# Optimization experiments

Hardware: AMD Instinct MI355X
Metric: run time of the kernel (lower is better)

## Reference

```python
import jax, jax.numpy as jnp
import numpy as np

N_NODES = 100000
N_EDGES = 1600000
IN_DIM = 128
HID = 128
HEADS = 8
NEG_SLOPE = 0.2  # PyG GATConv default


def _gat_layer(x, src, dst, W, a_src, a_dst, bias, heads, n_nodes):
    """One PyG-style GATConv (concat=True). src/dst already include self-loops."""
    out_ch = W.shape[1] // heads
    h = (x @ W).reshape(n_nodes, heads, out_ch)          # [N, H, C]
    alpha_s = jnp.sum(h * a_src, axis=-1)                # [N, H]
    alpha_d = jnp.sum(h * a_dst, axis=-1)                # [N, H]
    e = jax.nn.leaky_relu(alpha_s[src] + alpha_d[dst], negative_slope=NEG_SLOPE)  # [E, H]
    # segment softmax over destination nodes (stable; self-loops guarantee nonempty segments)
    m = jax.lax.stop_gradient(jax.ops.segment_max(e, dst, num_segments=n_nodes))
    ex = jnp.exp(e - m[dst])
    s = jax.ops.segment_sum(ex, dst, num_segments=n_nodes)
    alpha = ex / s[dst]                                  # [E, H]
    msg = h[src] * alpha[:, :, None]                     # [E, H, C]
    out = jax.ops.segment_sum(msg, dst, num_segments=n_nodes)  # [N, H, C]
    return out.reshape(n_nodes, heads * out_ch) + bias


def setup_inputs() -> dict:
    key = jax.random.key(0)
    ks = jax.random.split(key, 12)
    c1 = HID // HEADS  # per-head channels of layer 1
    g = lambda k, shape, fan_in: jax.random.normal(k, shape, dtype=jnp.float32) * (1.0 / np.sqrt(fan_in))
    return {
        "x": jax.random.normal(ks[0], (N_NODES, IN_DIM), dtype=jnp.float32),
        "edge_index": jax.random.randint(ks[1], (2, N_EDGES), 0, N_NODES, dtype=jnp.int32),
        "W1": g(ks[2], (IN_DIM, HEADS * c1), IN_DIM),
        "a_src1": g(ks[3], (HEADS, c1), c1),
        "a_dst1": g(ks[4], (HEADS, c1), c1),
        "b1": jnp.zeros((HEADS * c1,), dtype=jnp.float32),
        "W2": g(ks[5], (HID, HID), HID),
        "a_src2": g(ks[6], (1, HID), HID),
        "a_dst2": g(ks[7], (1, HID), HID),
        "b2": jnp.zeros((HID,), dtype=jnp.float32),
    }


def reference(x, edge_index, W1, a_src1, a_dst1, b1, W2, a_src2, a_dst2, b2):
    n = x.shape[0]
    loops = jnp.arange(n, dtype=edge_index.dtype)  # add_self_loops=True (PyG default)
    src = jnp.concatenate([edge_index[0], loops])
    dst = jnp.concatenate([edge_index[1], loops])
    h = _gat_layer(x, src, dst, W1, a_src1, a_dst1, b1, HEADS, n)
    h = jax.nn.elu(h)  # inter-layer ELU; dropout p=0.0 is a no-op
    out = _gat_layer(h, src, dst, W2, a_src2, a_dst2, b2, 1, n)
    return out
```

## Files before the change

kernel.cpp:

```cpp
#include <hip/hip_runtime.h>
#include <hip/hip_bf16.h>
#include <math.h>

#define NEG_SLOPE 0.2f

typedef _Float16 half8 __attribute__((ext_vector_type(8)));
typedef _Float16 half4 __attribute__((ext_vector_type(4)));
typedef _Float16 half2v __attribute__((ext_vector_type(2)));
typedef float f32x4 __attribute__((ext_vector_type(4)));

__device__ __forceinline__ float lrelu(float x){ return fmaxf(x, NEG_SLOPE * x); }

__global__ void hist_kernel(const int* __restrict__ dst, int E,
                            int* __restrict__ deg, int rangeSize){
  const int x   = blockIdx.x & 7;
  const int gb  = blockIdx.x >> 3;
  const int nGB = gridDim.x >> 3;
  const int lo = x * rangeSize, hi = lo + rangeSize;
  const int stride = nGB * blockDim.x;
  for (int i = gb * blockDim.x + threadIdx.x; i < E; i += stride){
    int d = dst[i];
    if (d >= lo && d < hi) atomicAdd(&deg[d], 1);
  }
}

__global__ void scan1_kernel(const int* __restrict__ deg, int N,
                             int* __restrict__ rowptr, int* __restrict__ bsum){
  __shared__ int sdata[256];
  int t = threadIdx.x;
  int base = blockIdx.x * 1024;
  int v[4];
  int run = 0;
#pragma unroll
  for (int j = 0; j < 4; ++j){
    int idx = base + t*4 + j;
    int d = (idx < N) ? deg[idx] : 0;
    run += d;
    v[j] = run;
  }
  sdata[t] = run;
  __syncthreads();
  for (int off = 1; off < 256; off <<= 1){
    int x = (t >= off) ? sdata[t - off] : 0;
    __syncthreads();
    sdata[t] += x;
    __syncthreads();
  }
  int prev = (t > 0) ? sdata[t-1] : 0;
#pragma unroll
  for (int j = 0; j < 4; ++j){
    int idx = base + t*4 + j;
    if (idx < N) rowptr[idx + 1] = v[j] + prev;
  }
  if (t == 255) bsum[blockIdx.x] = sdata[255];
}

__global__ void scan2_kernel(int* __restrict__ bsum, int nb){
  if (threadIdx.x == 0 && blockIdx.x == 0){
    int run = 0;
    for (int i = 0; i < nb; ++i){ int x = bsum[i]; bsum[i] = run; run += x; }
  }
}

__global__ void scan3_kernel(int* __restrict__ rowptr, const int* __restrict__ bsum,
                             int* __restrict__ cursor, int N){
  int i = blockIdx.x * blockDim.x + threadIdx.x;
  if (i == 0){ rowptr[0] = 0; cursor[0] = 0; }
  if (i < N){
    int v = rowptr[i + 1] + bsum[i >> 10];
    rowptr[i + 1] = v;
    cursor[i + 1] = v;
  }
}

__global__ void scatter_kernel(const int* __restrict__ src, const int* __restrict__ dst, int E,
                               int* __restrict__ cursor, int* __restrict__ csr_src, int rangeSize){
  const int x   = blockIdx.x & 7;
  const int gb  = blockIdx.x >> 3;
  const int nGB = gridDim.x >> 3;
  const int lo = x * rangeSize, hi = lo + rangeSize;
  const int stride = nGB * blockDim.x;
  for (int i = gb * blockDim.x + threadIdx.x; i < E; i += stride){
    int d = dst[i];
    if (d >= lo && d < hi){
      int pos = atomicAdd(&cursor[d], 1);
      csr_src[pos] = src[i];
    }
  }
}

__global__ void prep_kernel(const float* __restrict__ W1, const float* __restrict__ W2,
                            const float* __restrict__ as2, const float* __restrict__ ad2,
                            _Float16* __restrict__ Wt1, _Float16* __restrict__ Wt2,
                            float* __restrict__ w2s, float* __restrict__ w2d){
  int t = threadIdx.x;
  if (blockIdx.x < 2){
    const float* W = blockIdx.x ? W2 : W1;
    _Float16* Wt = blockIdx.x ? Wt2 : Wt1;
    for (int i = 0; i < 64; ++i){
      int e = i*256 + t;
      int k = e >> 7, c = e & 127;
      Wt[c*128 + k] = (_Float16)W[e];
    }
  } else {
    if (t < 128){
      float ps = 0.f, pd = 0.f;
      for (int c = 0; c < 128; ++c){
        float w = W2[t*128 + c];
        ps += w * as2[c];
        pd += w * ad2[c];
      }
      w2s[t] = ps;
      w2d[t] = pd;
    }
  }
}

template<int ALPHA_H, bool CASTF32, bool OUTF32>
__launch_bounds__(256, 2)
__global__ void gemm_mfma(const void* __restrict__ Aptr, const _Float16* __restrict__ Wt,
                          void* __restrict__ outp, const float* __restrict__ bias,
                          const float* __restrict__ a_src, const float* __restrict__ a_dst,
                          float* __restrict__ alpha_s, float* __restrict__ alpha_d, int N){
  __shared__ __align__(16) _Float16 Xs[128*128];
  __shared__ __align__(16) _Float16 Ws[128*128];
  __shared__ float apart[2][128][2];
  const int t = threadIdx.x;
  const int lane = t & 63;
  const int w = t >> 6;
  const int wr = w & 1, wc = w >> 1;
  const int rowBase = blockIdx.x * 128;
  const int lrow = lane & 15, lk = lane >> 4;

  if (CASTF32){
    const float* A = (const float*)Aptr;
#pragma unroll
    for (int p = 0; p < 16; ++p){
      int flat = p*256 + t;
      int row = flat >> 5, seg = flat & 31;
      int gr = rowBase + row;
      float4 v = (gr < N) ? *(const float4*)(A + (size_t)gr*128 + seg*4)
                          : make_float4(0.f,0.f,0.f,0.f);
      half4 hv = {(_Float16)v.x, (_Float16)v.y, (_Float16)v.z, (_Float16)v.w};
      int byt = (row*256 + seg*8) ^ ((row & 7) << 4);
      *(half4*)((char*)Xs + byt) = hv;
    }
  } else {
    const _Float16* A = (const _Float16*)Aptr;
#pragma unroll
    for (int p = 0; p < 8; ++p){
      int flat = p*256 + t;
      int row = flat >> 4, seg = flat & 15;
      int gr = rowBase + row;
      int4 v = (gr < N) ? *(const int4*)(A + (size_t)gr*128 + seg*8)
                        : make_int4(0,0,0,0);
      int byt = (row*256 + seg*16) ^ ((row & 7) << 4);
      *(int4*)((char*)Xs + byt) = v;
    }
  }
#pragma unroll
  for (int p = 0; p < 8; ++p){
    int flat = p*256 + t;
    int row = flat >> 4, seg = flat & 15;
    int4 v = *(const int4*)(Wt + row*128 + seg*8);
    int byt = (row*256 + seg*16) ^ ((row & 7) << 4);
    *(int4*)((char*)Ws + byt) = v;
  }
  __syncthreads();

  f32x4 acc[4][4];
#pragma unroll
  for (int mf = 0; mf < 4; ++mf)
#pragma unroll
    for (int nf = 0; nf < 4; ++nf) acc[mf][nf] = (f32x4){0.f,0.f,0.f,0.f};

#pragma unroll
  for (int ks = 0; ks < 4; ++ks){
    const int kbyte = ks*64 + lk*16;
    half8 b[4], a[4];
#pragma unroll
    for (int nf = 0; nf < 4; ++nf){
      int row = wr*64 + nf*16 + lrow;
      b[nf] = *(const half8*)((const char*)Xs + ((row*256 + kbyte) ^ ((row & 7) << 4)));
    }
#pragma unroll
    for (int mf = 0; mf < 4; ++mf){
      int col = wc*64 + mf*16 + lrow;
      a[mf] = *(const half8*)((const char*)Ws + ((col*256 + kbyte) ^ ((col & 7) << 4)));
    }
#pragma unroll
    for (int mf = 0; mf < 4; ++mf)
#pragma unroll
      for (int nf = 0; nf < 4; ++nf)
        acc[mf][nf] = __builtin_amdgcn_mfma_f32_16x16x32_f16(a[mf], b[nf], acc[mf][nf], 0, 0, 0);
  }

  if (OUTF32){
    float* outf = (float*)outp;
    float4 b4[4];
#pragma unroll
    for (int mf = 0; mf < 4; ++mf)
      b4[mf] = *(const float4*)(bias + wc*64 + mf*16 + lk*4);
#pragma unroll
    for (int nf = 0; nf < 4; ++nf){
      int row = rowBase + wr*64 + nf*16 + lrow;
      if (row < N){
#pragma unroll
        for (int mf = 0; mf < 4; ++mf){
          int col = wc*64 + mf*16 + lk*4;
          f32x4 v = acc[mf][nf];
          float4 st = make_float4(v.x + b4[mf].x, v.y + b4[mf].y, v.z + b4[mf].z, v.w + b4[mf].w);
          *(float4*)(outf + (size_t)row*128 + col) = st;
        }
      }
    }
  } else {
    _Float16* hout = (_Float16*)outp;
#pragma unroll
    for (int nf = 0; nf < 4; ++nf){
      int row = rowBase + wr*64 + nf*16 + lrow;
      if (row < N){
#pragma unroll
        for (int mf = 0; mf < 4; ++mf){
          int col = wc*64 + mf*16 + lk*4;
          f32x4 v = acc[mf][nf];
          half4 hv = {(_Float16)v.x, (_Float16)v.y, (_Float16)v.z, (_Float16)v.w};
          *(half4*)(hout + (size_t)row*128 + col) = hv;
        }
      }
    }
  }

  if (ALPHA_H > 0){
    float4 as4[4], ad4[4];
#pragma unroll
    for (int mf = 0; mf < 4; ++mf){
      int cb = wc*64 + mf*16 + lk*4;
      as4[mf] = *(const float4*)(a_src + cb);
      ad4[mf] = *(const float4*)(a_dst + cb);
    }
    if (ALPHA_H == 8){
#pragma unroll
      for (int nf = 0; nf < 4; ++nf){
        int row = rowBase + wr*64 + nf*16 + lrow;
#pragma unroll
        for (int mf = 0; mf < 4; ++mf){
          f32x4 v = acc[mf][nf];
          float ps = v.x*as4[mf].x + v.y*as4[mf].y + v.z*as4[mf].z + v.w*as4[mf].w;
          float pd = v.x*ad4[mf].x + v.y*ad4[mf].y + v.z*ad4[mf].z + v.w*ad4[mf].w;
          ps += __shfl_xor(ps, 16); ps += __shfl_xor(ps, 32);
          pd += __shfl_xor(pd, 16); pd += __shfl_xor(pd, 32);
          if (lane < 16 && row < N){
            int head = wc*4 + mf;
            alpha_s[(size_t)row*8 + head] = ps;
            alpha_d[(size_t)row*8 + head] = pd;
          }
        }
      }
    } else {
#pragma unroll
      for (int nf = 0; nf < 4; ++nf){
        float ps = 0.f, pd = 0.f;
#pragma unroll
        for (int mf = 0; mf < 4; ++mf){
          f32x4 v = acc[mf][nf];
          ps += v.x*as4[mf].x + v.y*as4[mf].y + v.z*as4[mf].z + v.w*as4[mf].w;
          pd += v.x*ad4[mf].x + v.y*ad4[mf].y + v.z*ad4[mf].z + v.w*ad4[mf].w;
        }
        ps += __shfl_xor(ps, 16); ps += __shfl_xor(ps, 32);
        pd += __shfl_xor(pd, 16); pd += __shfl_xor(pd, 32);
        if (lane < 16){
          int rl = wr*64 + nf*16 + lane;
          apart[0][rl][wc] = ps;
          apart[1][rl][wc] = pd;
        }
      }
      __syncthreads();
      if (wc == 0){
        int rl = wr*64 + lane;
        int row = rowBase + rl;
        if (row < N){
          alpha_s[row] = apart[0][rl][0] + apart[0][rl][1];
          alpha_d[row] = apart[1][rl][0] + apart[1][rl][1];
        }
      }
    }
  }
}

template<int H, bool LAYER1>
__launch_bounds__(256)
__global__ void agg_kernel(const _Float16* __restrict__ hb, const float* __restrict__ alpha_s,
                           const float* __restrict__ alpha_d,
                           const int* __restrict__ rowptr, const int* __restrict__ csr_src,
                           const float* __restrict__ bias,
                           const float* __restrict__ w2s, const float* __restrict__ w2d,
                           _Float16* __restrict__ outh,
                           float* __restrict__ as2, float* __restrict__ ad2, int N){
  const int wid = threadIdx.x >> 6, lane = threadIdx.x & 63;
  const int n = blockIdx.x * 4 + wid;
  if (n >= N) return;
  const int start = rowptr[n];
  const int deg = rowptr[n + 1] - start;
  const int T = deg + 1;

  const int g  = lane >> 4;
  const int l  = lane & 15;
  const int ch = l * 8;
  const int hm = (H == 8) ? (l >> 1) : 0;

  const int p1e = (H == 8) ? (lane >> 3) : lane;
  const int p1h = (H == 8) ? (lane & 7) : 0;
  const int CH  = (H == 8) ? 8 : 64;

  const float ad1 = alpha_d[(size_t)n*H + p1h];

  float acc[8];
#pragma unroll
  for (int k = 0; k < 8; ++k) acc[k] = 0.f;
  float ssum_l = 0.f;

  for (int base = 0; base < T; base += CH){
    int j = base + p1e;
    float exf = 0.f;
    int sv = n;
    if (j < T){
      if (j < deg) sv = csr_src[start + j];
      float e = alpha_s[(size_t)sv*H + p1h] + ad1;
      e = fmaxf(e, NEG_SLOPE * e);
      exf = __expf(e);
      ssum_l += exf;
    }
    int lim  = min(CH, T - base);
    int limr = (lim + 3) & ~3;
    for (int jj = g; jj < limr; jj += 4){
      int srcl = (H == 8) ? (jj*8 + hm) : jj;
      int s = __shfl(sv, srcl);
      float ex = __shfl(exf, srcl);
      int4 hv = *(const int4*)(hb + (s << 7) + ch);
      half2v h0 = __builtin_bit_cast(half2v, hv.x);
      half2v h1 = __builtin_bit_cast(half2v, hv.y);
      half2v h2 = __builtin_bit_cast(half2v, hv.z);
      half2v h3 = __builtin_bit_cast(half2v, hv.w);
      acc[0] += (float)h0.x * ex; acc[1] += (float)h0.y * ex;
      acc[2] += (float)h1.x * ex; acc[3] += (float)h1.y * ex;
      acc[4] += (float)h2.x * ex; acc[5] += (float)h2.y * ex;
      acc[6] += (float)h3.x * ex; acc[7] += (float)h3.y * ex;
    }
  }

  if (H == 8){
    ssum_l += __shfl_xor(ssum_l, 8);
    ssum_l += __shfl_xor(ssum_l, 16);
    ssum_l += __shfl_xor(ssum_l, 32);
  } else {
#pragma unroll
    for (int off = 1; off < 64; off <<= 1) ssum_l += __shfl_xor(ssum_l, off);
  }
  float ssum = __shfl(ssum_l, hm);

#pragma unroll
  for (int k = 0; k < 8; ++k){
    acc[k] += __shfl_xor(acc[k], 16);
    acc[k] += __shfl_xor(acc[k], 32);
  }

  if (lane < 16){
    float inv = 1.0f / ssum;
    float o[8];
#pragma unroll
    for (int k = 0; k < 8; ++k) o[k] = acc[k] * inv;
    if (LAYER1){
      float4 b0 = *(const float4*)(bias + ch);
      float4 b1 = *(const float4*)(bias + ch + 4);
      float bb[8] = {b0.x,b0.y,b0.z,b0.w,b1.x,b1.y,b1.z,b1.w};
#pragma unroll
      for (int k = 0; k < 8; ++k){
        float v = o[k] + bb[k];
        o[k] = (v > 0.f) ? v : expm1f(v);
      }
    }
    half8 ho;
#pragma unroll
    for (int k = 0; k < 8; ++k) ho[k] = (_Float16)o[k];
    *(half8*)(outh + (size_t)n*128 + ch) = ho;

    if (LAYER1){
      float4 s0 = *(const float4*)(w2s + ch);
      float4 s1 = *(const float4*)(w2s + ch + 4);
      float4 d0 = *(const float4*)(w2d + ch);
      float4 d1 = *(const float4*)(w2d + ch + 4);
      float ps = o[0]*s0.x + o[1]*s0.y + o[2]*s0.z + o[3]*s0.w
               + o[4]*s1.x + o[5]*s1.y + o[6]*s1.z + o[7]*s1.w;
      float pd = o[0]*d0.x + o[1]*d0.y + o[2]*d0.z + o[3]*d0.w
               + o[4]*d1.x + o[5]*d1.y + o[6]*d1.z + o[7]*d1.w;
#pragma unroll
      for (int off = 1; off < 16; off <<= 1){
        ps += __shfl_xor(ps, off);
        pd += __shfl_xor(pd, off);
      }
      if (l == 0){
        as2[n] = ps;
        ad2[n] = pd;
      }
    }
  }
}

extern "C" void kernel_launch(void* const* d_in, const int* in_sizes, int n_in,
                              void* d_out, int out_size, void* d_ws, size_t ws_size,
                              hipStream_t stream){
  const float* x      = (const float*)d_in[0];
  const int*   ei     = (const int*)  d_in[1];
  const float* W1     = (const float*)d_in[2];
  const float* a_src1 = (const float*)d_in[3];
  const float* a_dst1 = (const float*)d_in[4];
  const float* b1     = (const float*)d_in[5];
  const float* W2     = (const float*)d_in[6];
  const float* a_src2 = (const float*)d_in[7];
  const float* a_dst2 = (const float*)d_in[8];
  const float* b2     = (const float*)d_in[9];
  float* out = (float*)d_out;

  const int N = in_sizes[0] / 128;
  const int E = in_sizes[1] / 2;
  const int* src = ei;
  const int* dst = ei + E;

  char* ws = (char*)d_ws;
  size_t off = 0;
  auto alloc = [&](size_t bytes) -> void* {
    void* p = ws + off;
    off += (bytes + 255) & ~(size_t)255;
    return p;
  };
  _Float16* hb   = (_Float16*)alloc((size_t)N * 128 * 2);
  _Float16* act  = (_Float16*)alloc((size_t)N * 128 * 2);
  float* asb     = (float*)alloc((size_t)N * 8 * 4);
  float* adb     = (float*)alloc((size_t)N * 8 * 4);
  float* as2     = (float*)alloc((size_t)N * 4);
  float* ad2     = (float*)alloc((size_t)N * 4);
  _Float16* Wt1  = (_Float16*)alloc(16384 * 2);
  _Float16* Wt2  = (_Float16*)alloc(16384 * 2);
  float* w2s     = (float*)alloc(128 * 4);
  float* w2d     = (float*)alloc(128 * 4);
  int*   csr     = (int*)  alloc((size_t)E * 4);
  int*   rowptr  = (int*)  alloc((size_t)(N + 1) * 4);
  int*   cursor  = (int*)  alloc((size_t)(N + 1) * 4);
  int*   deg     = (int*)  alloc((size_t)N * 4);
  int*   bsum    = (int*)  alloc(4096);

  hipMemsetAsync(deg, 0, (size_t)N * 4, stream);

  const int nb = (N + 1023) / 1024;
  const int rangeSize = (N + 7) / 8;
  prep_kernel   <<<3, 256, 0, stream>>>(W1, W2, a_src2, a_dst2, Wt1, Wt2, w2s, w2d);
  hist_kernel   <<<2048, 256, 0, stream>>>(dst, E, deg, rangeSize);
  scan1_kernel  <<<nb, 256, 0, stream>>>(deg, N, rowptr, bsum);
  scan2_kernel  <<<1, 64, 0, stream>>>(bsum, nb);
  scan3_kernel  <<<(N + 255)/256, 256, 0, stream>>>(rowptr, bsum, cursor, N);
  scatter_kernel<<<2048, 256, 0, stream>>>(src, dst, E, cursor, csr, rangeSize);

  const int gBlocks  = (N + 127) / 128;
  const int nBlocks4 = (N + 3) / 4;

  gemm_mfma<8, true, false><<<gBlocks, 256, 0, stream>>>(
      x, Wt1, hb, nullptr, a_src1, a_dst1, asb, adb, N);
  agg_kernel<8, true><<<nBlocks4, 256, 0, stream>>>(
      hb, asb, adb, rowptr, csr, b1, w2s, w2d, act, as2, ad2, N);
  agg_kernel<1, false><<<nBlocks4, 256, 0, stream>>>(
      act, as2, ad2, rowptr, csr, nullptr, nullptr, nullptr, hb, nullptr, nullptr, N);
  gemm_mfma<0, false, true><<<gBlocks, 256, 0, stream>>>(
      hb, Wt2, out, b2, nullptr, nullptr, nullptr, nullptr, N);
}
```

Baseline: 390.5 us.

## Compute attention weights per lane directly and unroll edge loop by four

The aggregation kernel stops computing edge exponentials cooperatively and broadcasting them with shuffles. Instead, each 16-lane group walks its own strided subset of edges, loads the source index and alpha_s for its head itself, computes the exponential, and accumulates it. The edge loop is unrolled four ways so index and alpha loads can be in flight together, and the softmax sum is reduced together with the accumulators. This removes shuffle traffic and the two-phase chunk structure, but repeats the exp and the alpha_s loads across lanes that share a head.

```diff
diff --git a/kernel.cpp b/kernel.cpp
--- a/kernel.cpp
+++ b/kernel.cpp
@@ -302,67 +302,63 @@
   if (n >= N) return;
   const int start = rowptr[n];
   const int deg = rowptr[n + 1] - start;
-  const int T = deg + 1;
 
   const int g  = lane >> 4;
   const int l  = lane & 15;
   const int ch = l * 8;
   const int hm = (H == 8) ? (l >> 1) : 0;
-
-  const int p1e = (H == 8) ? (lane >> 3) : lane;
-  const int p1h = (H == 8) ? (lane & 7) : 0;
-  const int CH  = (H == 8) ? 8 : 64;
-
-  const float ad1 = alpha_d[(size_t)n*H + p1h];
+  const float ad_m = alpha_d[(size_t)n*H + hm];
 
   float acc[8];
 #pragma unroll
   for (int k = 0; k < 8; ++k) acc[k] = 0.f;
-  float ssum_l = 0.f;
-
-  for (int base = 0; base < T; base += CH){
-    int j = base + p1e;
-    float exf = 0.f;
-    int sv = n;
-    if (j < T){
-      if (j < deg) sv = csr_src[start + j];
-      float e = alpha_s[(size_t)sv*H + p1h] + ad1;
-      e = fmaxf(e, NEG_SLOPE * e);
-      exf = __expf(e);
-      ssum_l += exf;
-    }
-    int lim  = min(CH, T - base);
-    int limr = (lim + 3) & ~3;
-    for (int jj = g; jj < limr; jj += 4){
-      int srcl = (H == 8) ? (jj*8 + hm) : jj;
-      int s = __shfl(sv, srcl);
-      float ex = __shfl(exf, srcl);
-      int4 hv = *(const int4*)(hb + (s << 7) + ch);
-      half2v h0 = __builtin_bit_cast(half2v, hv.x);
-      half2v h1 = __builtin_bit_cast(half2v, hv.y);
-      half2v h2 = __builtin_bit_cast(half2v, hv.z);
-      half2v h3 = __builtin_bit_cast(half2v, hv.w);
-      acc[0] += (float)h0.x * ex; acc[1] += (float)h0.y * ex;
-      acc[2] += (float)h1.x * ex; acc[3] += (float)h1.y * ex;
-      acc[4] += (float)h2.x * ex; acc[5] += (float)h2.y * ex;
-      acc[6] += (float)h3.x * ex; acc[7] += (float)h3.y * ex;
-    }
-  }
-
-  if (H == 8){
-    ssum_l += __shfl_xor(ssum_l, 8);
-    ssum_l += __shfl_xor(ssum_l, 16);
-    ssum_l += __shfl_xor(ssum_l, 32);
-  } else {
-#pragma unroll
-    for (int off = 1; off < 64; off <<= 1) ssum_l += __shfl_xor(ssum_l, off);
-  }
-  float ssum = __shfl(ssum_l, hm);
-
-#pragma unroll
-  for (int k = 0; k < 8; ++k){
-    acc[k] += __shfl_xor(acc[k], 16);
-    acc[k] += __shfl_xor(acc[k], 32);
+  float ssum = 0.f;
+
+  auto edge = [&](int s, float ex){
+    int4 hv = *(const int4*)(hb + ((size_t)s << 7) + ch);
+    half2v h0 = __builtin_bit_cast(half2v, hv.x);
+    half2v h1 = __builtin_bit_cast(half2v, hv.y);
+    half2v h2 = __builtin_bit_cast(half2v, hv.z);
+    half2v h3 = __builtin_bit_cast(half2v, hv.w);
+    acc[0] += (float)h0.x * ex; acc[1] += (float)h0.y * ex;
+    acc[2] += (float)h1.x * ex; acc[3] += (float)h1.y * ex;
+    acc[4] += (float)h2.x * ex; acc[5] += (float)h2.y * ex;
+    acc[6] += (float)h3.x * ex; acc[7] += (float)h3.y * ex;
+    ssum += ex;
+  };
+
+  if (g == 3){
+    float ex = __expf(lrelu(alpha_s[(size_t)n*H + hm] + ad_m));
+    edge(n, ex);
+  }
+
+  int i = g;
+  for (; i + 12 < deg; i += 16){
+    int s0 = csr_src[start + i];
+    int s1 = csr_src[start + i + 4];
+    int s2 = csr_src[start + i + 8];
+    int s3 = csr_src[start + i + 12];
+    float a0 = alpha_s[(size_t)s0*H + hm];
+    float a1 = alpha_s[(size_t)s1*H + hm];
+    float a2 = alpha_s[(size_t)s2*H + hm];
+    float a3 = alpha_s[(size_t)s3*H + hm];
+    float e0 = __expf(lrelu(a0 + ad_m));
+    float e1 = __expf(lrelu(a1 + ad_m));
+    float e2 = __expf(lrelu(a2 + ad_m));
+    float e3 = __expf(lrelu(a3 + ad_m));
+    edge(s0, e0); edge(s1, e1); edge(s2, e2); edge(s3, e3);
+  }
+  for (; i < deg; i += 4){
+    int s0 = csr_src[start + i];
+    float e0 = __expf(lrelu(alpha_s[(size_t)s0*H + hm] + ad_m));
+    edge(s0, e0);
+  }
+
+#pragma unroll
+  for (int off = 16; off < 64; off <<= 1){
+    ssum += __shfl_xor(ssum, off);
+#pragma unroll
+    for (int k = 0; k < 8; ++k) acc[k] += __shfl_xor(acc[k], off);
   }
 
   if (lane < 16){
```

After: 375.5 us. 1.04x faster.
